# Kernel optimization log

Hardware: AMD Instinct MI355X
Metric: run time of the kernel (lower is better)

The kernel has to match this reference:

```python
import jax, jax.numpy as jnp
import numpy as np

N = 100000   # nodes
E = 400000   # edges (before self-loops)
G = 4000     # graphs in batch
F_IN = 32    # node_embedding
HID = 128    # hidden_channels
H = 3        # heads (hard-coded in module)
W3 = H * HID # 384, post-concat width
NC = 10      # num_classes
NL = 4       # num_layers
NEG_SLOPE = 0.2


def _lin(key, fan_in, fan_out):
    return jax.random.normal(key, (fan_in, fan_out), jnp.float32) * (1.0 / np.sqrt(fan_in))


def setup_inputs() -> dict:
    key = jax.random.key(0)
    ks = iter(jax.random.split(key, 40))
    x = jax.random.normal(next(ks), (N, F_IN), jnp.float32)
    edge_index = jax.random.randint(next(ks), (2, E), 0, N, dtype=jnp.int32)
    batch = jnp.sort(jax.random.randint(next(ks), (N,), 0, G, dtype=jnp.int32))
    inp = dict(x=x, edge_index=edge_index, batch=batch)
    # MLP stem
    inp['lin1_w'] = _lin(next(ks), F_IN, 2 * HID); inp['lin1_b'] = jnp.zeros((2 * HID,), jnp.float32)
    inp['lin2_w'] = _lin(next(ks), 2 * HID, HID);  inp['lin2_b'] = jnp.zeros((HID,), jnp.float32)
    # conv1: GATConv(HID -> HID, heads=3)
    inp['w0'] = _lin(next(ks), HID, W3)
    inp['as0'] = jax.random.normal(next(ks), (H, HID), jnp.float32) * 0.1
    inp['ad0'] = jax.random.normal(next(ks), (H, HID), jnp.float32) * 0.1
    inp['b0'] = jnp.zeros((W3,), jnp.float32)
    # remaining NL-1 convs: GATConv(W3 -> HID, heads=3), stacked
    inp['wl'] = jnp.stack([_lin(next(ks), W3, W3) for _ in range(NL - 1)])
    inp['asl'] = jax.random.normal(next(ks), (NL - 1, H, HID), jnp.float32) * 0.1
    inp['adl'] = jax.random.normal(next(ks), (NL - 1, H, HID), jnp.float32) * 0.1
    inp['bl'] = jnp.zeros((NL - 1, W3), jnp.float32)
    # batch norms (NL total, all width W3)
    inp['gamma'] = jnp.ones((NL, W3), jnp.float32)
    inp['beta'] = jnp.zeros((NL, W3), jnp.float32)
    # head
    inp['lin3_w'] = _lin(next(ks), W3, HID); inp['lin3_b'] = jnp.zeros((HID,), jnp.float32)
    inp['lin4_w'] = _lin(next(ks), HID, NC); inp['lin4_b'] = jnp.zeros((NC,), jnp.float32)
    return inp


def _gat(x, W, a_src, a_dst, bias, src, dst):
    # PyG GATConv, concat heads. x: [N, Fin]
    h = (x @ W).reshape(N, H, HID)                       # [N, H, C]
    es = jnp.einsum('nhc,hc->nh', h, a_src)              # [N, H]
    ed = jnp.einsum('nhc,hc->nh', h, a_dst)
    e = jax.nn.leaky_relu(es[src] + ed[dst], NEG_SLOPE)  # [Etot, H]
    m = jax.ops.segment_max(e, dst, num_segments=N)      # segment softmax over incoming edges
    p = jnp.exp(e - m[dst])
    s = jax.ops.segment_sum(p, dst, num_segments=N)
    alpha = p / s[dst]                                   # every node has a self-loop -> s>0
    out = jax.ops.segment_sum(alpha[:, :, None] * h[src], dst, num_segments=N)
    return out.reshape(N, W3) + bias


def _bn(x, g, b):
    mu = x.mean(0)
    var = x.var(0)
    return (x - mu) * jax.lax.rsqrt(var + 1e-5) * g + b


def reference(x, edge_index, batch, lin1_w, lin1_b, lin2_w, lin2_b,
              w0, as0, ad0, b0, wl, asl, adl, bl, gamma, beta,
              lin3_w, lin3_b, lin4_w, lin4_b):
    loop = jnp.arange(N, dtype=edge_index.dtype)
    src = jnp.concatenate([edge_index[0], loop])  # add_self_loops=True (PyG default)
    dst = jnp.concatenate([edge_index[1], loop])
    h = jax.nn.relu(x @ lin1_w + lin1_b)
    h = jax.nn.relu(h @ lin2_w + lin2_b)
    h = _gat(h, w0, as0, ad0, b0, src, dst)
    h = _bn(h, gamma[0], beta[0])
    for i in range(NL - 1):
        h = _gat(h, wl[i], asl[i], adl[i], bl[i], src, dst)
        h = _bn(h, gamma[i + 1], beta[i + 1])
    # global mean pool over graphs
    sums = jax.ops.segment_sum(h, batch, num_segments=G)
    cnt = jax.ops.segment_sum(jnp.ones((N,), h.dtype), batch, num_segments=G)
    g = sums / jnp.maximum(cnt, 1.0)[:, None]
    g = jax.nn.relu(g @ lin3_w + lin3_b)
    logits = g @ lin4_w + lin4_b
    return jax.nn.log_softmax(logits, axis=-1)
```

## Files before the change

### kernel.cpp

```cpp
#include <hip/hip_runtime.h>

#define NN      100000
#define NN2     100096
#define NE      400000
#define ETOT    500000
#define NG      4000
#define W3D     384
#define HIDD    128
#define NCLS    10
#define NSLICE  256

typedef unsigned short u16;
typedef unsigned int   u32;
typedef unsigned long long u64;
typedef __attribute__((ext_vector_type(8))) short short8;
typedef __attribute__((ext_vector_type(4))) float f32x4;

static __device__ __forceinline__ float bf2f(u16 u) {
  return __uint_as_float(((u32)u) << 16);
}
static __device__ __forceinline__ float bflo(u32 u) {
  return __uint_as_float(u << 16);
}
static __device__ __forceinline__ float bfhi(u32 u) {
  return __uint_as_float(u & 0xffff0000u);
}
static __device__ __forceinline__ u16 f2b(float f) {
  u32 u = __float_as_uint(f);
  u32 r = (u + 0x7fffu + ((u >> 16) & 1u)) >> 16;
  return (u16)r;
}

static __device__ __forceinline__ void llds16(const u16* g, u16* l) {
  __builtin_amdgcn_global_load_lds(
      (const __attribute__((address_space(1))) void*)(u64)(const void*)g,
      (__attribute__((address_space(3))) void*)(u64)(void*)l, 16, 0, 0);
}

__global__ void mg_zero_out(float* out, int n) {
  int i = blockIdx.x * 256 + threadIdx.x;
  if (i < n) out[i] = 0.f;
}

__global__ void mg_cvt_x(const float* __restrict__ x, u16* __restrict__ Xb) {
  int idx = blockIdx.x * 256 + threadIdx.x;
  if (idx >= NN2 * 64) return;
  int row = idx >> 6, col = idx & 63;
  Xb[idx] = (row < NN && col < 32) ? f2b(x[row * 32 + col]) : (u16)0;
}

__global__ void mg_transpose_pad(const float* __restrict__ in, u16* __restrict__ out,
                                 int K, int Nn, int Kpad) {
  int idx = blockIdx.x * 256 + threadIdx.x;
  if (idx >= Nn * Kpad) return;
  int n = idx / Kpad, k = idx - n * Kpad;
  out[idx] = (k < K) ? f2b(in[k * Nn + n]) : (u16)0;
}

__global__ void mg_fold_w(const u16* __restrict__ Wt, const float* __restrict__ scale,
                          const float* __restrict__ shift, u16* __restrict__ Wp,
                          float* __restrict__ bp) {
  __shared__ float red[128];
  int j = blockIdx.x, t = threadIdx.x;
  const u16* src = Wt + (size_t)j * W3D;
  u16* dst = Wp + (size_t)j * W3D;
  float acc = 0.f;
  for (int k = t; k < W3D; k += 128) {
    float w = bf2f(src[k]);
    dst[k] = f2b(w * scale[k]);
    acc += w * shift[k];
  }
  red[t] = acc; __syncthreads();
  for (int off = 64; off; off >>= 1) {
    if (t < off) red[t] += red[t + off];
    __syncthreads();
  }
  if (t == 0) bp[j] = red[0];
}

__global__ void mg_edge_histo(const int* __restrict__ ei, int* __restrict__ deg) {
  int e = blockIdx.x * 256 + threadIdx.x;
  if (e >= ETOT) return;
  int d = (e < NE) ? ei[NE + e] : (e - NE);
  atomicAdd(&deg[d], 1);
}

__global__ void mg_scan1(const int* __restrict__ in, int* __restrict__ bsum, int n) {
  __shared__ int sd[256];
  int tid = threadIdx.x;
  int base = blockIdx.x * 1024 + tid * 4;
  int s = 0;
#pragma unroll
  for (int j = 0; j < 4; ++j) { int i = base + j; if (i < n) s += in[i]; }
  sd[tid] = s; __syncthreads();
  for (int off = 128; off > 0; off >>= 1) {
    if (tid < off) sd[tid] += sd[tid + off];
    __syncthreads();
  }
  if (tid == 0) bsum[blockIdx.x] = sd[0];
}

__global__ void mg_scan2(int* __restrict__ bsum, int nb) {
  __shared__ int sd[256];
  int tid = threadIdx.x;
  int v = (tid < nb) ? bsum[tid] : 0;
  sd[tid] = v; __syncthreads();
  for (int off = 1; off < 256; off <<= 1) {
    int t = (tid >= off) ? sd[tid - off] : 0;
    __syncthreads();
    sd[tid] += t;
    __syncthreads();
  }
  if (tid < nb) bsum[tid] = sd[tid] - v;
}

__global__ void mg_scan3(const int* __restrict__ in, const int* __restrict__ bexcl,
                         int* __restrict__ out, int n) {
  __shared__ int sd[256];
  int tid = threadIdx.x;
  int base = blockIdx.x * 1024 + tid * 4;
  int loc[4]; int s = 0;
#pragma unroll
  for (int j = 0; j < 4; ++j) { int i = base + j; loc[j] = (i < n) ? in[i] : 0; s += loc[j]; }
  sd[tid] = s; __syncthreads();
  for (int off = 1; off < 256; off <<= 1) {
    int t = (tid >= off) ? sd[tid - off] : 0;
    __syncthreads();
    sd[tid] += t;
    __syncthreads();
  }
  int run = sd[tid] - s + bexcl[blockIdx.x];
#pragma unroll
  for (int j = 0; j < 4; ++j) {
    int i = base + j;
    if (i < n) { out[i] = run; run += loc[j]; if (i == n - 1) out[n] = run; }
  }
}

__global__ void mg_edge_scatter(const int* __restrict__ ei, int* __restrict__ fill,
                                int* __restrict__ colsrc) {
  int e = blockIdx.x * 256 + threadIdx.x;
  if (e >= ETOT) return;
  int s, d;
  if (e < NE) { s = ei[e]; d = ei[NE + e]; } else { s = e - NE; d = s; }
  int pos = atomicAdd(&fill[d], 1);
  colsrc[pos] = s;
}

__global__ void mg_graph_ptr(const int* __restrict__ batch, int* __restrict__ gptr) {
  int g = blockIdx.x * 256 + threadIdx.x;
  if (g > NG) return;
  if (g == NG) { gptr[NG] = NN; return; }
  int lo = 0, hi = NN;
  while (lo < hi) { int mid = (lo + hi) >> 1; if (batch[mid] < g) lo = mid + 1; else hi = mid; }
  gptr[g] = lo;
}

#define GBM 128
#define GBN 128
#define GBK 64
#define CP  136

__global__ __launch_bounds__(256) void mg_gemm(
    const u16* __restrict__ Ag, const u16* __restrict__ Bt,
    int Mstore, int Nn, int K,
    u16* __restrict__ Cb, const float* __restrict__ bias, int relu,
    const float* __restrict__ asrc, const float* __restrict__ adst,
    float* __restrict__ aes, float* __restrict__ aed) {
  __shared__ u16 lds[32768];
  int tid = threadIdx.x;
  int n0 = blockIdx.x * GBN, m0 = blockIdx.y * GBM;
  int lane = tid & 63, wv = tid >> 6;
  int mw = (wv & 1) * 64, nw = (wv >> 1) * 64;
  int lr = lane & 15, lq = lane >> 4;
  int sr = lane & 7, scl = lane >> 3;

  f32x4 acc[4][4];
#pragma unroll
  for (int mi = 0; mi < 4; ++mi)
#pragma unroll
    for (int ni = 0; ni < 4; ++ni) acc[mi][ni] = (f32x4){0.f, 0.f, 0.f, 0.f};

  const u16* aB = Ag + (size_t)m0 * K + scl * 8;
  const u16* bB = Bt + (size_t)n0 * K + scl * 8;
  int niter = K / GBK;

#pragma unroll
  for (int j = 0; j < 4; ++j) {
    int g = wv * 4 + j, grow = g * 8 + sr;
    llds16(aB + (size_t)grow * K, lds + g * 512);
    llds16(bB + (size_t)grow * K, lds + 16384 + g * 512);
  }

  for (int it = 0; it < niter; ++it) {
    __syncthreads();
    if (it + 1 < niter) {
      int k0 = (it + 1) * GBK, b = (it + 1) & 1;
#pragma unroll
      for (int j = 0; j < 4; ++j) {
        int g = wv * 4 + j, grow = g * 8 + sr;
        llds16(aB + (size_t)grow * K + k0, lds + b * 8192 + g * 512);
        llds16(bB + (size_t)grow * K + k0, lds + 16384 + b * 8192 + g * 512);
      }
    }
    const u16* Al = lds + (it & 1) * 8192;
    const u16* Bl = lds + 16384 + (it & 1) * 8192;
#pragma unroll
    for (int kk = 0; kk < GBK; kk += 32) {
      int ca = (kk >> 3) + lq;
      short8 af[4], bfr[4];
#pragma unroll
      for (int mi = 0; mi < 4; ++mi) {
        int r = mw + mi * 16 + lr;
        af[mi] = *(const short8*)(Al + (r >> 3) * 512 + ca * 64 + (r & 7) * 8);
      }
#pragma unroll
      for (int ni = 0; ni < 4; ++ni) {
        int r = nw + ni * 16 + lr;
        bfr[ni] = *(const short8*)(Bl + (r >> 3) * 512 + ca * 64 + (r & 7) * 8);
      }
#pragma unroll
      for (int mi = 0; mi < 4; ++mi)
#pragma unroll
        for (int ni = 0; ni < 4; ++ni)
          acc[mi][ni] = __builtin_amdgcn_mfma_f32_16x16x32_bf16(af[mi], bfr[ni], acc[mi][ni], 0, 0, 0);
    }
    __syncthreads();
  }

  float bvv[4];
#pragma unroll
  for (int ni = 0; ni < 4; ++ni)
    bvv[ni] = bias ? bias[n0 + nw + ni * 16 + lr] : 0.f;

#pragma unroll
  for (int mi = 0; mi < 4; ++mi)
#pragma unroll
    for (int ni = 0; ni < 4; ++ni) {
      int cl = nw + ni * 16 + lr;
      int rb = mw + mi * 16 + lq * 4;
#pragma unroll
      for (int r = 0; r < 4; ++r) {
        float v = acc[mi][ni][r] + bvv[ni];
        if (relu) v = fmaxf(v, 0.f);
        lds[(rb + r) * CP + cl] = f2b(v);
      }
    }
  __syncthreads();

  int rowl = tid >> 1, half = (tid & 1) * 64;
  const u16* src = lds + rowl * CP + half;
  uint4 creg[8];
#pragma unroll
  for (int j = 0; j < 8; ++j) creg[j] = *(const uint4*)(src + j * 8);
  u16* gout = Cb + (size_t)(m0 + rowl) * Nn + n0 + half;
#pragma unroll
  for (int j = 0; j < 8; ++j) *(uint4*)(gout + j * 8) = creg[j];

  if (aes) {
    const float* ap = asrc + n0 + half;
    const float* dp = adst + n0 + half;
    float se = 0.f, de = 0.f;
#pragma unroll
    for (int j = 0; j < 8; ++j) {
      float4 a0 = *(const float4*)(ap + j * 8);
      float4 a1 = *(const float4*)(ap + j * 8 + 4);
      float4 d0 = *(const float4*)(dp + j * 8);
      float4 d1 = *(const float4*)(dp + j * 8 + 4);
      uint4 rv = creg[j];
      float v0 = bflo(rv.x), v1 = bfhi(rv.x), v2 = bflo(rv.y), v3 = bfhi(rv.y);
      float v4 = bflo(rv.z), v5 = bfhi(rv.z), v6 = bflo(rv.w), v7 = bfhi(rv.w);
      se += v0 * a0.x + v1 * a0.y + v2 * a0.z + v3 * a0.w
          + v4 * a1.x + v5 * a1.y + v6 * a1.z + v7 * a1.w;
      de += v0 * d0.x + v1 * d0.y + v2 * d0.z + v3 * d0.w
          + v4 * d1.x + v5 * d1.y + v6 * d1.z + v7 * d1.w;
    }
    se += __shfl_xor(se, 1);
    de += __shfl_xor(de, 1);
    int row = m0 + rowl;
    if ((tid & 1) == 0 && row < Mstore) {
      aes[row * 4 + blockIdx.x] = se;
      aed[row * 4 + blockIdx.x] = de;
    }
  }
}

__global__ __launch_bounds__(256) void mg_aggregate(
    const u16* __restrict__ B, const float* __restrict__ es,
    const float* __restrict__ ed, const int* __restrict__ rowptr,
    const int* __restrict__ colsrc, const float* __restrict__ bias,
    u16* __restrict__ A, float* __restrict__ stats) {
  __shared__ float buf[4 * W3D];
  int wv = threadIdx.x >> 6, lane = threadIdx.x & 63;
  int n = blockIdx.x * 4 + wv;
  if (n < NN) {
    int r0 = rowptr[n], r1 = rowptr[n + 1];
    float4 edv = *(const float4*)(ed + 4 * n);
    float m0v = -1e30f, m1v = -1e30f, m2v = -1e30f;
    for (int r = r0 + lane; r < r1; r += 64) {
      int s = colsrc[r];
      float4 ev = *(const float4*)(es + 4 * s);
      float e0 = ev.x + edv.x; e0 = (e0 > 0.f) ? e0 : 0.2f * e0;
      float e1 = ev.y + edv.y; e1 = (e1 > 0.f) ? e1 : 0.2f * e1;
      float e2 = ev.z + edv.z; e2 = (e2 > 0.f) ? e2 : 0.2f * e2;
      m0v = fmaxf(m0v, e0); m1v = fmaxf(m1v, e1); m2v = fmaxf(m2v, e2);
    }
#pragma unroll
    for (int off = 32; off; off >>= 1) {
      m0v = fmaxf(m0v, __shfl_xor(m0v, off));
      m1v = fmaxf(m1v, __shfl_xor(m1v, off));
      m2v = fmaxf(m2v, __shfl_xor(m2v, off));
    }
    if (lane < 48) {
      int h = lane >> 4;
      float mh  = (h == 0) ? m0v  : ((h == 1) ? m1v  : m2v);
      float edh = (h == 0) ? edv.x : ((h == 1) ? edv.y : edv.z);
      float accv[8];
#pragma unroll
      for (int j = 0; j < 8; ++j) accv[j] = 0.f;
      float ssum = 0.f;
      int c = lane * 8;
      int sN = colsrc[r0];
      float4 evN = *(const float4*)(es + 4 * sN);
      uint4 rvN = *(const uint4*)(B + (size_t)sN * W3D + c);
      for (int r = r0; r < r1; ++r) {
        float4 ev = evN; uint4 rv = rvN;
        if (r + 1 < r1) {
          sN = colsrc[r + 1];
          evN = *(const float4*)(es + 4 * sN);
          rvN = *(const uint4*)(B + (size_t)sN * W3D + c);
        }
        float e = ((h == 0) ? ev.x : ((h == 1) ? ev.y : ev.z)) + edh;
        e = (e > 0.f) ? e : 0.2f * e;
        float p = __expf(e - mh);
        ssum += p;
        accv[0] += p * bflo(rv.x); accv[1] += p * bfhi(rv.x);
        accv[2] += p * bflo(rv.y); accv[3] += p * bfhi(rv.y);
        accv[4] += p * bflo(rv.z); accv[5] += p * bfhi(rv.z);
        accv[6] += p * bflo(rv.w); accv[7] += p * bfhi(rv.w);
      }
      float inv = 1.0f / ssum;
      float4 bv0 = *(const float4*)(bias + c);
      float4 bv1 = *(const float4*)(bias + c + 4);
      float v[8];
      v[0] = accv[0] * inv + bv0.x; v[1] = accv[1] * inv + bv0.y;
      v[2] = accv[2] * inv + bv0.z; v[3] = accv[3] * inv + bv0.w;
      v[4] = accv[4] * inv + bv1.x; v[5] = accv[5] * inv + bv1.y;
      v[6] = accv[6] * inv + bv1.z; v[7] = accv[7] * inv + bv1.w;
      uint4 st;
      st.x = (u32)f2b(v[0]) | ((u32)f2b(v[1]) << 16);
      st.y = (u32)f2b(v[2]) | ((u32)f2b(v[3]) << 16);
      st.z = (u32)f2b(v[4]) | ((u32)f2b(v[5]) << 16);
      st.w = (u32)f2b(v[6]) | ((u32)f2b(v[7]) << 16);
      *(uint4*)(A + (size_t)n * W3D + c) = st;
      *(float4*)(buf + wv * W3D + c)     = (float4){v[0], v[1], v[2], v[3]};
      *(float4*)(buf + wv * W3D + c + 4) = (float4){v[4], v[5], v[6], v[7]};
    }
  } else if (lane < 48) {
    int c = lane * 8;
    *(float4*)(buf + wv * W3D + c)     = (float4){0.f, 0.f, 0.f, 0.f};
    *(float4*)(buf + wv * W3D + c + 4) = (float4){0.f, 0.f, 0.f, 0.f};
  }
  __syncthreads();
  for (int t = threadIdx.x; t < W3D; t += 256) {
    float s = 0.f, q = 0.f;
#pragma unroll
    for (int w = 0; w < 4; ++w) {
      float x = buf[w * W3D + t];
      s += x; q += x * x;
    }
    float* sl = stats + (size_t)(blockIdx.x & (NSLICE - 1)) * 768;
    atomicAdd(&sl[t], s);
    atomicAdd(&sl[W3D + t], q);
  }
}

__global__ void mg_bn_finalize(const float* __restrict__ stats, const float* __restrict__ gamma,
                               const float* __restrict__ beta, float* __restrict__ scale,
                               float* __restrict__ shift) {
  int c = threadIdx.x;
  float s = 0.f, q = 0.f;
  for (int b = 0; b < NSLICE; ++b) { s += stats[b * 768 + c]; q += stats[b * 768 + W3D + c]; }
  const float invN = 1.0f / (float)NN;
  float mu = s * invN;
  float var = fmaxf(q * invN - mu * mu, 0.f);
  float inv = rsqrtf(var + 1e-5f);
  float g = gamma[c], be = beta[c];
  scale[c] = g * inv;
  shift[c] = be - mu * g * inv;
}

__global__ void mg_pool(const u16* __restrict__ A, const float* __restrict__ scale,
                        const float* __restrict__ shift, const int* __restrict__ gptr,
                        float* __restrict__ pooled) {
  int g = blockIdx.x, c = threadIdx.x;
  int r0 = gptr[g], r1 = gptr[g + 1];
  float acc = 0.f;
  for (int n = r0; n < r1; ++n) acc += bf2f(A[(size_t)n * W3D + c]);
  int cnt = r1 - r0;
  float v = (cnt > 0) ? (acc / (float)cnt) * scale[c] + shift[c] : 0.f;
  pooled[g * W3D + c] = v;
}

__global__ void mg_head(const float* __restrict__ pooled, const float* __restrict__ w3,
                        const float* __restrict__ b3, const float* __restrict__ w4,
                        const float* __restrict__ b4, float* __restrict__ out) {
  __shared__ float p[W3D];
  __shared__ float g2[HIDD];
  __shared__ float lg[NCLS];
  int g = blockIdx.x, t = threadIdx.x;
  for (int i = t; i < W3D; i += 128) p[i] = pooled[g * W3D + i];
  __syncthreads();
  float acc = 0.f;
  for (int k = 0; k < W3D; ++k) acc += p[k] * w3[k * HIDD + t];
  g2[t] = fmaxf(acc + b3[t], 0.f);
  __syncthreads();
  if (t < NCLS) {
    float a = 0.f;
    for (int k = 0; k < HIDD; ++k) a += g2[k] * w4[k * NCLS + t];
    lg[t] = a + b4[t];
  }
  __syncthreads();
  if (t < NCLS) {
    float m = -1e30f;
#pragma unroll
    for (int j = 0; j < NCLS; ++j) m = fmaxf(m, lg[j]);
    float se = 0.f;
#pragma unroll
    for (int j = 0; j < NCLS; ++j) se += __expf(lg[j] - m);
    out[g * NCLS + t] = lg[t] - m - __logf(se);
  }
}

extern "C" void kernel_launch(void* const* d_in, const int* in_sizes, int n_in,
                              void* d_out, int out_size, void* d_ws, size_t ws_size,
                              hipStream_t stream) {
  const float* x     = (const float*)d_in[0];
  const int*   ei    = (const int*)d_in[1];
  const int*   batch = (const int*)d_in[2];
  const float* w1    = (const float*)d_in[3];
  const float* b1    = (const float*)d_in[4];
  const float* w2    = (const float*)d_in[5];
  const float* b2    = (const float*)d_in[6];
  const float* w0    = (const float*)d_in[7];
  const float* as0   = (const float*)d_in[8];
  const float* ad0   = (const float*)d_in[9];
  const float* b0    = (const float*)d_in[10];
  const float* wl    = (const float*)d_in[11];
  const float* asl   = (const float*)d_in[12];
  const float* adl   = (const float*)d_in[13];
  const float* bl    = (const float*)d_in[14];
  const float* gamma = (const float*)d_in[15];
  const float* beta  = (const float*)d_in[16];
  const float* w3    = (const float*)d_in[17];
  const float* b3    = (const float*)d_in[18];
  const float* w4    = (const float*)d_in[19];
  const float* b4    = (const float*)d_in[20];
  float* out = (float*)d_out;

  char* w = (char*)d_ws;
  auto alloc = [&](size_t bytes) -> void* {
    void* p = (void*)w;
    w += (bytes + 255) & ~(size_t)255;
    return p;
  };
  u16*   P      = (u16*)alloc((size_t)NN2 * W3D * 2);
  u16*   Q      = (u16*)alloc((size_t)NN2 * W3D * 2);
  float* es     = (float*)alloc((size_t)NN * 4 * 4);
  float* ed     = (float*)alloc((size_t)NN * 4 * 4);
  int*   deg    = (int*)alloc((size_t)NN * 4);
  int*   rowptr = (int*)alloc((size_t)(NN + 1) * 4);
  int*   fill   = (int*)alloc((size_t)NN * 4);
  int*   colsrc = (int*)alloc((size_t)ETOT * 4);
  int*   bsum   = (int*)alloc(256 * 4);
  float* stats  = (float*)alloc((size_t)NSLICE * 768 * 4);
  float* scale  = (float*)alloc(W3D * 4);
  float* shift  = (float*)alloc(W3D * 4);
  float* bprime = (float*)alloc(W3D * 4);
  int*   gptr   = (int*)alloc((size_t)(NG + 1) * 4);
  float* pooled = (float*)alloc((size_t)NG * W3D * 4);
  u16*   W1T    = (u16*)alloc(256 * 64 * 2);
  u16*   W2T    = (u16*)alloc(128 * 256 * 2);
  u16*   W0T    = (u16*)alloc(384 * 128 * 2);
  u16*   WlT    = (u16*)alloc((size_t)3 * 384 * 384 * 2);
  u16*   WpT    = (u16*)alloc((size_t)384 * 384 * 2);
  u16*   Xb     = Q;

  if ((size_t)(w - (char*)d_ws) > ws_size) {
    mg_zero_out<<<(out_size + 255) / 256, 256, 0, stream>>>(out, out_size);
    return;
  }

  mg_cvt_x<<<(NN2 * 64 + 255) / 256, 256, 0, stream>>>(x, Xb);
  mg_transpose_pad<<<(256 * 64 + 255) / 256, 256, 0, stream>>>(w1, W1T, 32, 256, 64);
  mg_transpose_pad<<<(128 * 256 + 255) / 256, 256, 0, stream>>>(w2, W2T, 256, 128, 256);
  mg_transpose_pad<<<(384 * 128 + 255) / 256, 256, 0, stream>>>(w0, W0T, 128, 384, 128);
  for (int i = 0; i < 3; ++i)
    mg_transpose_pad<<<(384 * 384 + 255) / 256, 256, 0, stream>>>(
        wl + (size_t)i * 384 * 384, WlT + (size_t)i * 384 * 384, 384, 384, 384);

  hipMemsetAsync(deg, 0, (size_t)NN * 4, stream);
  mg_edge_histo<<<(ETOT + 255) / 256, 256, 0, stream>>>(ei, deg);
  int nb = (NN + 1023) / 1024;
  mg_scan1<<<nb, 256, 0, stream>>>(deg, bsum, NN);
  mg_scan2<<<1, 256, 0, stream>>>(bsum, nb);
  mg_scan3<<<nb, 256, 0, stream>>>(deg, bsum, rowptr, NN);
  hipMemcpyAsync(fill, rowptr, (size_t)NN * 4, hipMemcpyDeviceToDevice, stream);
  mg_edge_scatter<<<(ETOT + 255) / 256, 256, 0, stream>>>(ei, fill, colsrc);
  mg_graph_ptr<<<(NG + 1 + 255) / 256, 256, 0, stream>>>(batch, gptr);

  dim3 blk(256);
  int mtiles = NN2 / GBM;

  mg_gemm<<<dim3(2, mtiles), blk, 0, stream>>>(Xb, W1T, NN, 256, 64,
                                               P, b1, 1,
                                               nullptr, nullptr, nullptr, nullptr);
  mg_gemm<<<dim3(1, mtiles), blk, 0, stream>>>(P, W2T, NN, 128, 256,
                                               Q, b2, 1,
                                               nullptr, nullptr, nullptr, nullptr);

  for (int i = 0; i < 4; ++i) {
    int K = (i == 0) ? 128 : 384;
    const u16* Bt;
    const float* bi_g = nullptr;
    if (i == 0) {
      Bt = W0T;
    } else {
      mg_fold_w<<<384, 128, 0, stream>>>(WlT + (size_t)(i - 1) * 384 * 384,
                                         scale, shift, WpT, bprime);
      Bt = WpT;
      bi_g = bprime;
    }
    const float* as = (i == 0) ? as0 : (asl + (size_t)(i - 1) * 384);
    const float* ad = (i == 0) ? ad0 : (adl + (size_t)(i - 1) * 384);
    const float* bi = (i == 0) ? b0  : (bl  + (size_t)(i - 1) * 384);
    hipMemsetAsync(stats, 0, (size_t)NSLICE * 768 * 4, stream);
    mg_gemm<<<dim3(3, mtiles), blk, 0, stream>>>(Q, Bt, NN, W3D, K,
                                                 P, bi_g, 0,
                                                 as, ad, es, ed);
    mg_aggregate<<<(NN + 3) / 4, blk, 0, stream>>>(P, es, ed, rowptr, colsrc, bi, Q, stats);
    mg_bn_finalize<<<1, 384, 0, stream>>>(stats, gamma + (size_t)i * W3D,
                                          beta + (size_t)i * W3D, scale, shift);
  }

  mg_pool<<<NG, 384, 0, stream>>>(Q, scale, shift, gptr, pooled);
  mg_head<<<NG, 128, 0, stream>>>(pooled, w3, b3, w4, b4, out);
}
```

Baseline: 1.181 ms.

## Drop max pass in GAT aggregation, use self-loop score as softmax shift

```diff
diff --git a/kernel.cpp b/kernel.cpp
--- a/kernel.cpp
+++ b/kernel.cpp
@@ -290,45 +290,48 @@
     const float* __restrict__ ed, const int* __restrict__ rowptr,
     const int* __restrict__ colsrc, const float* __restrict__ bias,
     u16* __restrict__ A, float* __restrict__ stats) {
-  __shared__ float buf[4 * W3D];
+  __shared__ float bS[4 * W3D];
+  __shared__ float bQ[4 * W3D];
   int wv = threadIdx.x >> 6, lane = threadIdx.x & 63;
-  int n = blockIdx.x * 4 + wv;
-  if (n < NN) {
-    int r0 = rowptr[n], r1 = rowptr[n + 1];
-    float4 edv = *(const float4*)(ed + 4 * n);
-    float m0v = -1e30f, m1v = -1e30f, m2v = -1e30f;
-    for (int r = r0 + lane; r < r1; r += 64) {
-      int s = colsrc[r];
-      float4 ev = *(const float4*)(es + 4 * s);
-      float e0 = ev.x + edv.x; e0 = (e0 > 0.f) ? e0 : 0.2f * e0;
-      float e1 = ev.y + edv.y; e1 = (e1 > 0.f) ? e1 : 0.2f * e1;
-      float e2 = ev.z + edv.z; e2 = (e2 > 0.f) ? e2 : 0.2f * e2;
-      m0v = fmaxf(m0v, e0); m1v = fmaxf(m1v, e1); m2v = fmaxf(m2v, e2);
-    }
-#pragma unroll
-    for (int off = 32; off; off >>= 1) {
-      m0v = fmaxf(m0v, __shfl_xor(m0v, off));
-      m1v = fmaxf(m1v, __shfl_xor(m1v, off));
-      m2v = fmaxf(m2v, __shfl_xor(m2v, off));
-    }
-    if (lane < 48) {
-      int h = lane >> 4;
-      float mh  = (h == 0) ? m0v  : ((h == 1) ? m1v  : m2v);
+  if (lane < 48) {
+    int h = lane >> 4;
+    int cc = lane * 8;
+    float4 bv0 = *(const float4*)(bias + cc);
+    float4 bv1 = *(const float4*)(bias + cc + 4);
+    float stS[8], stQ[8];
+#pragma unroll
+    for (int j = 0; j < 8; ++j) { stS[j] = 0.f; stQ[j] = 0.f; }
+#pragma unroll
+    for (int sub = 0; sub < 2; ++sub) {
+      int n = blockIdx.x * 8 + wv * 2 + sub;
+      int r0 = rowptr[n], r1 = rowptr[n + 1];
+      float4 edv = *(const float4*)(ed + 4 * n);
+      float4 esn = *(const float4*)(es + 4 * n);
+      float s0 = esn.x + edv.x; s0 = (s0 > 0.f) ? s0 : 0.2f * s0;
+      float s1 = esn.y + edv.y; s1 = (s1 > 0.f) ? s1 : 0.2f * s1;
+      float s2 = esn.z + edv.z; s2 = (s2 > 0.f) ? s2 : 0.2f * s2;
+      float mh  = (h == 0) ? s0 : ((h == 1) ? s1 : s2);
       float edh = (h == 0) ? edv.x : ((h == 1) ? edv.y : edv.z);
       float accv[8];
 #pragma unroll
       for (int j = 0; j < 8; ++j) accv[j] = 0.f;
       float ssum = 0.f;
-      int c = lane * 8;
-      int sN = colsrc[r0];
-      float4 evN = *(const float4*)(es + 4 * sN);
-      uint4 rvN = *(const uint4*)(B + (size_t)sN * W3D + c);
+      int sA = __builtin_amdgcn_readfirstlane(colsrc[r0]);
+      float4 evA = *(const float4*)(es + 4 * sA);
+      uint4  rvA = *(const uint4*)(B + (size_t)sA * W3D + cc);
+      float4 evB = evA; uint4 rvB = rvA;
+      if (r0 + 1 < r1) {
+        int sB = __builtin_amdgcn_readfirstlane(colsrc[r0 + 1]);
+        evB = *(const float4*)(es + 4 * sB);
+        rvB = *(const uint4*)(B + (size_t)sB * W3D + cc);
+      }
       for (int r = r0; r < r1; ++r) {
-        float4 ev = evN; uint4 rv = rvN;
-        if (r + 1 < r1) {
-          sN = colsrc[r + 1];
-          evN = *(const float4*)(es + 4 * sN);
-          rvN = *(const uint4*)(B + (size_t)sN * W3D + c);
+        float4 ev = evA; uint4 rv = rvA;
+        evA = evB; rvA = rvB;
+        if (r + 2 < r1) {
+          int sC = __builtin_amdgcn_readfirstlane(colsrc[r + 2]);
+          evB = *(const float4*)(es + 4 * sC);
+          rvB = *(const uint4*)(B + (size_t)sC * W3D + cc);
         }
         float e = ((h == 0) ? ev.x : ((h == 1) ? ev.y : ev.z)) + edh;
         e = (e > 0.f) ? e : 0.2f * e;
@@ -340,8 +343,6 @@
         accv[6] += p * bflo(rv.w); accv[7] += p * bfhi(rv.w);
       }
       float inv = 1.0f / ssum;
-      float4 bv0 = *(const float4*)(bias + c);
-      float4 bv1 = *(const float4*)(bias + c + 4);
       float v[8];
       v[0] = accv[0] * inv + bv0.x; v[1] = accv[1] * inv + bv0.y;
       v[2] = accv[2] * inv + bv0.z; v[3] = accv[3] * inv + bv0.w;
@@ -352,23 +353,20 @@
       st.y = (u32)f2b(v[2]) | ((u32)f2b(v[3]) << 16);
       st.z = (u32)f2b(v[4]) | ((u32)f2b(v[5]) << 16);
       st.w = (u32)f2b(v[6]) | ((u32)f2b(v[7]) << 16);
-      *(uint4*)(A + (size_t)n * W3D + c) = st;
-      *(float4*)(buf + wv * W3D + c)     = (float4){v[0], v[1], v[2], v[3]};
-      *(float4*)(buf + wv * W3D + c + 4) = (float4){v[4], v[5], v[6], v[7]};
-    }
-  } else if (lane < 48) {
-    int c = lane * 8;
-    *(float4*)(buf + wv * W3D + c)     = (float4){0.f, 0.f, 0.f, 0.f};
-    *(float4*)(buf + wv * W3D + c + 4) = (float4){0.f, 0.f, 0.f, 0.f};
+      *(uint4*)(A + (size_t)n * W3D + cc) = st;
+#pragma unroll
+      for (int j = 0; j < 8; ++j) { stS[j] += v[j]; stQ[j] += v[j] * v[j]; }
+    }
+    *(float4*)(bS + wv * W3D + cc)     = (float4){stS[0], stS[1], stS[2], stS[3]};
+    *(float4*)(bS + wv * W3D + cc + 4) = (float4){stS[4], stS[5], stS[6], stS[7]};
+    *(float4*)(bQ + wv * W3D + cc)     = (float4){stQ[0], stQ[1], stQ[2], stQ[3]};
+    *(float4*)(bQ + wv * W3D + cc + 4) = (float4){stQ[4], stQ[5], stQ[6], stQ[7]};
   }
   __syncthreads();
   for (int t = threadIdx.x; t < W3D; t += 256) {
     float s = 0.f, q = 0.f;
 #pragma unroll
-    for (int w = 0; w < 4; ++w) {
-      float x = buf[w * W3D + t];
-      s += x; q += x * x;
-    }
+    for (int w = 0; w < 4; ++w) { s += bS[w * W3D + t]; q += bQ[w * W3D + t]; }
     float* sl = stats + (size_t)(blockIdx.x & (NSLICE - 1)) * 768;
     atomicAdd(&sl[t], s);
     atomicAdd(&sl[W3D + t], q);
@@ -538,7 +536,7 @@
     mg_gemm<<<dim3(3, mtiles), blk, 0, stream>>>(Q, Bt, NN, W3D, K,
                                                  P, bi_g, 0,
                                                  as, ad, es, ed);
-    mg_aggregate<<<(NN + 3) / 4, blk, 0, stream>>>(P, es, ed, rowptr, colsrc, bi, Q, stats);
+    mg_aggregate<<<NN / 8, blk, 0, stream>>>(P, es, ed, rowptr, colsrc, bi, Q, stats);
     mg_bn_finalize<<<1, 384, 0, stream>>>(stats, gamma + (size_t)i * W3D,
                                           beta + (size_t)i * W3D, scale, shift);
   }
```

Measured after the change: 1.117 ms. 5.4% less time.
